# Kernel optimization log

Measured on AMD Instinct MI355X. Metric: run time of the kernel, lower is better.

The kernel has to match this reference:

```python
import jax, jax.numpy as jnp
import numpy as np

T, B, I, H = 512, 64, 512, 512

def _glorot(key, shape):
    fan_in, fan_out = shape
    std = np.sqrt(2.0 / (fan_in + fan_out))
    return (jax.random.normal(key, shape, dtype=jnp.float32) * std)

def setup_inputs() -> dict:
    key = jax.random.key(0)
    ks = jax.random.split(key, 9)
    inp = {"X": jax.random.normal(ks[0], (T, B, I), dtype=jnp.float32)}
    names = ["Wa_x", "Wi_x", "Wf_x", "Wo_x"]
    for n, k in zip(names, ks[1:5]):
        inp[n] = _glorot(k, (I, H))
    names_h = ["Wa_h", "Wi_h", "Wf_h", "Wo_h"]
    for n, k in zip(names_h, ks[5:9]):
        inp[n] = _glorot(k, (H, H))
    for n in ["ba", "bi", "bf", "bo"]:
        inp[n] = jnp.zeros((H,), dtype=jnp.float32)
    return inp

def reference(X, Wa_x, Wi_x, Wf_x, Wo_x, Wa_h, Wi_h, Wf_h, Wo_h, ba, bi, bf, bo):
    # Precompute input projections for all timesteps: [T,B,H] each
    Xa = jnp.einsum('tbi,ih->tbh', X, Wa_x) + ba
    Xi = jnp.einsum('tbi,ih->tbh', X, Wi_x) + bi
    Xf = jnp.einsum('tbi,ih->tbh', X, Wf_x) + bf
    Xo = jnp.einsum('tbi,ih->tbh', X, Wo_x) + bo

    def step(carry, xt):
        h, s = carry
        xa, xi, xf, xo = xt
        # At t=0 h=0 and s=0, which matches the original's special-cased first step
        a = jnp.tanh(xa + h @ Wa_h)
        i = jax.nn.sigmoid(xi + h @ Wi_h)
        f = jax.nn.sigmoid(xf + h @ Wf_h)
        o = jax.nn.sigmoid(xo + h @ Wo_h)
        s_new = a * i + s * f
        h_new = jnp.tanh(s_new) * o
        return (h_new, s_new), h_new

    h0 = jnp.zeros((B, H), dtype=X.dtype)
    s0 = jnp.zeros((B, H), dtype=X.dtype)
    _, hs = jax.lax.scan(step, (h0, s0), (Xa, Xi, Xf, Xo))
    return hs  # [T, B, H] (return_sequences=True)
```

## Files before the change

### kernel.cpp

```cpp
#include <hip/hip_runtime.h>
#include <cmath>


typedef __attribute__((ext_vector_type(8)))  short   short8;
typedef __attribute__((ext_vector_type(4)))  short   short4v;
typedef __attribute__((ext_vector_type(4)))  float   f32x4;
typedef __attribute__((ext_vector_type(16))) float   f32x16;

#define TSTEPS 512

__device__ __forceinline__ unsigned short f2bf(float f) {
  unsigned u = __builtin_bit_cast(unsigned, f);
  unsigned r = (u + 0x7FFFu + ((u >> 16) & 1u)) >> 16;
  return (unsigned short)r;
}
__device__ __forceinline__ float bf2f(unsigned short s) {
  unsigned u = ((unsigned)s) << 16;
  return __builtin_bit_cast(float, u);
}
__device__ __forceinline__ void gload_lds16(const void* g, void* l) {
  __builtin_amdgcn_global_load_lds(
      (const __attribute__((address_space(1))) unsigned int*)g,
      (__attribute__((address_space(3))) unsigned int*)l, 16, 0, 0);
}
__device__ __forceinline__ float sigmoid_fast(float x) {
  return 1.0f / (1.0f + __expf(-x));
}
__device__ __forceinline__ float tanh_fast(float x) {
  float e = __expf(2.0f * x);
  return 1.0f - 2.0f / (e + 1.0f);
}

__global__ __launch_bounds__(256) void prep_wT(
    const float* __restrict__ Wax, const float* __restrict__ Wix,
    const float* __restrict__ Wfx, const float* __restrict__ Wox,
    const float* __restrict__ Wah, const float* __restrict__ Wih,
    const float* __restrict__ Wfh, const float* __restrict__ Woh,
    unsigned short* __restrict__ WxT, unsigned short* __restrict__ WhT) {
  __shared__ float tile[32][33];
  int bx = blockIdx.x;
  int mat = bx >> 8;
  int t32 = bx & 255;
  int k0 = (t32 & 15) * 32;
  int h0 = (t32 >> 4) * 32;
  const float* S =
      (mat == 0) ? Wax : (mat == 1) ? Wix : (mat == 2) ? Wfx :
      (mat == 3) ? Wox : (mat == 4) ? Wah : (mat == 5) ? Wih :
      (mat == 6) ? Wfh : Woh;
  unsigned short* D = (mat < 4) ? WxT : WhT;
  int g = mat & 3;
  int tx = threadIdx.x & 31, ty = threadIdx.x >> 5;
#pragma unroll
  for (int r = 0; r < 4; ++r)
    tile[ty + r * 8][tx] = S[(size_t)(k0 + ty + r * 8) * 512 + h0 + tx];
  __syncthreads();
#pragma unroll
  for (int r = 0; r < 4; ++r) {
    int h = h0 + ty + r * 8;
    int k = k0 + tx;
    D[((size_t)(g * 512 + h) << 9) + k] = f2bf(tile[tx][ty + r * 8]);
  }
}

__global__ __launch_bounds__(256) void prep_xbf(const float* __restrict__ X,
                                                unsigned short* __restrict__ Xbf) {
  size_t i = (size_t)blockIdx.x * 256 + threadIdx.x;
  f32x4 v = *(const f32x4*)(X + i * 4);
  short4v o;
  o[0] = (short)f2bf(v[0]); o[1] = (short)f2bf(v[1]);
  o[2] = (short)f2bf(v[2]); o[3] = (short)f2bf(v[3]);
  *(short4v*)(Xbf + i * 4) = o;
}

__global__ __launch_bounds__(256) void prep_bias(
    const float* __restrict__ ba, const float* __restrict__ bi,
    const float* __restrict__ bf, const float* __restrict__ bo,
    float* __restrict__ biascat) {
  int n = blockIdx.x * 256 + threadIdx.x;
  int g = n >> 9, h = n & 511;
  const float* s = (g == 0) ? ba : (g == 1) ? bi : (g == 2) ? bf : bo;
  biascat[n] = s[h];
}

__global__ __launch_bounds__(256, 1) void lstm_fused(
    const unsigned short* __restrict__ Xbf,
    const unsigned short* __restrict__ WxT,
    const float* __restrict__ bcat,
    unsigned short* __restrict__ Xg,
    const unsigned short* __restrict__ WhT,
    unsigned short* __restrict__ hbuf,
    int* __restrict__ flags,
    int* __restrict__ xcnt,
    float* __restrict__ out) {
  __shared__ unsigned short smem[32768];
  const int tid = threadIdx.x;
  const int w = tid >> 6, l = tid & 63;

  if (blockIdx.x >= 32) {
    unsigned short* Asm_ = smem;
    unsigned short* Bsm_ = smem + 8192;
    const int wkr = blockIdx.x - 32;
    const int wm = (w >> 1) * 64, wn = (w & 1) * 64;
#pragma unroll 1
    for (int id = wkr; id < 4096; id += 512) {
      const int mt = id >> 4, nt = id & 15;
      const int m0 = mt * 128, n0 = nt * 128;
      f32x4 acc[4][4] = {};
      for (int ks = 0; ks < 8; ++ks) {
        int k0 = ks * 64;
        __syncthreads();
        int lr = l >> 3;
        int ksl = ((l & 7) ^ lr) * 8;
#pragma unroll
        for (int ii = 0; ii < 4; ++ii) {
          int i = w * 4 + ii;
          int r = i * 8 + lr;
          gload_lds16(Xbf + (size_t)(m0 + r) * 512 + k0 + ksl,
                      Asm_ + i * 512 + l * 8);
        }
#pragma unroll
        for (int ii = 0; ii < 4; ++ii) {
          int i = w * 4 + ii;
          int r = i * 8 + lr;
          gload_lds16(WxT + (size_t)(n0 + r) * 512 + k0 + ksl,
                      Bsm_ + i * 512 + l * 8);
        }
        __syncthreads();
#pragma unroll
        for (int kk = 0; kk < 2; ++kk) {
          short8 af[4], bfr[4];
#pragma unroll
          for (int mi = 0; mi < 4; ++mi) {
            int row = wm + mi * 16 + (l & 15);
            int slot = (kk * 4 + (l >> 4)) ^ (row & 7);
            af[mi] = *(const short8*)(Asm_ + row * 64 + slot * 8);
          }
#pragma unroll
          for (int ni = 0; ni < 4; ++ni) {
            int row = wn + ni * 16 + (l & 15);
            int slot = (kk * 4 + (l >> 4)) ^ (row & 7);
            bfr[ni] = *(const short8*)(Bsm_ + row * 64 + slot * 8);
          }
#pragma unroll
          for (int mi = 0; mi < 4; ++mi)
#pragma unroll
            for (int ni = 0; ni < 4; ++ni)
              acc[mi][ni] = __builtin_amdgcn_mfma_f32_16x16x32_bf16(
                  af[mi], bfr[ni], acc[mi][ni], 0, 0, 0);
        }
      }
#pragma unroll
      for (int mi = 0; mi < 4; ++mi)
#pragma unroll
        for (int ni = 0; ni < 4; ++ni) {
          int col = n0 + wn + ni * 16 + (l & 15);
          float bias = bcat[col];
          int g = col >> 9, h = col & 511;
          int chunk = h >> 3, e = h & 7;
#pragma unroll
          for (int r = 0; r < 4; ++r) {
            int m = m0 + wm + mi * 16 + (l >> 4) * 4 + r;
            int tt = m >> 6, bb = m & 63;
            unsigned off =
                (unsigned)(((((tt * 4 + g) * 64 + chunk) * 64 + bb) * 8 + e) * 2);
            unsigned val = (unsigned)f2bf(acc[mi][ni][r] + bias);
            asm volatile("global_store_short %0, %1, %2 sc0 sc1"
                         :: "v"(off), "v"(val), "s"(Xg) : "memory");
          }
        }
      asm volatile("s_waitcnt vmcnt(0)" ::: "memory");
      __syncthreads();
      if (tid == 0)
        __hip_atomic_fetch_add(xcnt + mt, 1, __ATOMIC_RELAXED,
                               __HIP_MEMORY_SCOPE_AGENT);
    }
    return;
  }

  unsigned short* hsm0 = smem;
  unsigned short* hsm1 = smem + 16384;
  const int j = blockIdx.x;
  const int mi = j & 1;
  const int cc = j >> 1;

  short8 wf[32];
  {
    const int m = l & 31;
    const int g = m >> 3;
    const int hcol_w = cc * 32 + w * 8 + (m & 7);
    const unsigned short* base =
        WhT + (((size_t)(g * 512 + hcol_w)) << 9) + (l >> 5) * 8;
#pragma unroll
    for (int kt = 0; kt < 32; ++kt) wf[kt] = *(const short8*)(base + kt * 16);
  }

  const int b = mi * 32 + (l & 31);
  const int half = l >> 5;
  const int hcol0 = cc * 32 + w * 8 + half * 4;
  const int mychunk = cc * 4 + w;

  const unsigned stg_goff0 = (unsigned)(half * 1024 + (mi * 32 + (l & 31)) * 16);
  const int stg_loff0 = w * 8192 + l * 16;
  const int ld_loff0 = half * 512 + (l & 31) * 16;
  const unsigned st_voff = (unsigned)(mychunk * 1024 + b * 16 + half * 8);

  int* const myflag = flags + (mi * 16 + cc) * 32;
  int* const pollflag = flags + (mi * 16 + (l & 15)) * 32;

  float s4[4] = {0.f, 0.f, 0.f, 0.f};

  uint2 xgn[4];
  int verified = 0;
  {
    int cv;
    do {
      cv = __hip_atomic_load(xcnt, __ATOMIC_RELAXED, __HIP_MEMORY_SCOPE_AGENT);
    } while (!__all(cv >= 16));
    asm volatile("" ::: "memory");
#pragma unroll
    for (int g = 0; g < 4; ++g)
      xgn[g] = *(const uint2*)(Xg +
          ((((size_t)(0 * 4 + g) * 64 + mychunk) * 64 + b) * 8 + half * 4));
  }

#pragma unroll 1
  for (int t = 0; t < TSTEPS; ++t) {
    f32x16 asum = {};
    if (t > 0) {
      int fv;
      do {
        fv = __hip_atomic_load(pollflag, __ATOMIC_RELAXED,
                               __HIP_MEMORY_SCOPE_AGENT);
      } while (!__all(fv >= t));
      asm volatile("" ::: "memory");
      const unsigned short* hbase = hbuf + (size_t)((t - 1) & 1) * 32768;
      unsigned short* hs = ((t - 1) & 1) ? hsm1 : hsm0;
      short8 tmp[8];
#pragma unroll
      for (int i = 0; i < 8; ++i) {
        asm volatile("global_load_dwordx4 %0, %1, %2 sc0 sc1"
                     : "=v"(tmp[i])
                     : "v"(stg_goff0 + (unsigned)((w * 8 + i) * 2048)),
                       "s"(hbase));
      }
      asm volatile("s_waitcnt vmcnt(0)" ::: "memory");
      __builtin_amdgcn_sched_barrier(0);
#pragma unroll
      for (int i = 0; i < 8; ++i)
        *(short8*)((char*)hs + stg_loff0 + i * 1024) = tmp[i];
      __syncthreads();
      f32x16 a0 = {}, a1 = {};
#pragma unroll
      for (int kt = 0; kt < 32; kt += 2) {
        short8 b0 = *(const short8*)((const char*)hs + ld_loff0 + kt * 1024);
        short8 b1 = *(const short8*)((const char*)hs + ld_loff0 + (kt + 1) * 1024);
        a0 = __builtin_amdgcn_mfma_f32_32x32x16_bf16(wf[kt], b0, a0, 0, 0, 0);
        a1 = __builtin_amdgcn_mfma_f32_32x32x16_bf16(wf[kt + 1], b1, a1,
                                                     0, 0, 0);
      }
      asum = a0 + a1;
    }
    float hout[4];
#pragma unroll
    for (int q = 0; q < 4; ++q) {
      float pa = asum[0 * 4 + q] + bf2f((unsigned short)((q < 2 ? xgn[0].x : xgn[0].y) >> ((q & 1) * 16)));
      float pi = asum[1 * 4 + q] + bf2f((unsigned short)((q < 2 ? xgn[1].x : xgn[1].y) >> ((q & 1) * 16)));
      float pf = asum[2 * 4 + q] + bf2f((unsigned short)((q < 2 ? xgn[2].x : xgn[2].y) >> ((q & 1) * 16)));
      float po = asum[3 * 4 + q] + bf2f((unsigned short)((q < 2 ? xgn[3].x : xgn[3].y) >> ((q & 1) * 16)));
      float a  = tanh_fast(pa);
      float ig = sigmoid_fast(pi);
      float fg = sigmoid_fast(pf);
      float og = sigmoid_fast(po);
      s4[q] = a * ig + s4[q] * fg;
      hout[q] = tanh_fast(s4[q]) * og;
    }
    {
      unsigned lo = (unsigned)f2bf(hout[0]) | ((unsigned)f2bf(hout[1]) << 16);
      unsigned hi = (unsigned)f2bf(hout[2]) | ((unsigned)f2bf(hout[3]) << 16);
      uint2 hd; hd.x = lo; hd.y = hi;
      const unsigned short* sbase = hbuf + (size_t)(t & 1) * 32768;
      asm volatile("global_store_dwordx2 %0, %1, %2 sc0 sc1"
                   :: "v"(st_voff), "v"(hd), "s"(sbase) : "memory");
      asm volatile("s_waitcnt vmcnt(0)" ::: "memory");
      __syncthreads();
      if (tid == 0)
        __hip_atomic_store(myflag, t + 1, __ATOMIC_RELAXED,
                           __HIP_MEMORY_SCOPE_AGENT);
    }
    f32x4 ov;
    ov[0] = hout[0]; ov[1] = hout[1]; ov[2] = hout[2]; ov[3] = hout[3];
    *(f32x4*)(out + ((size_t)t * 64 + b) * 512 + hcol0) = ov;
    const int tn = (t + 1 < TSTEPS) ? t + 1 : TSTEPS - 1;
    const int mtn = tn >> 1;
    if (mtn > verified) {
      int cv;
      do {
        cv = __hip_atomic_load(xcnt + mtn, __ATOMIC_RELAXED,
                               __HIP_MEMORY_SCOPE_AGENT);
      } while (!__all(cv >= 16));
      asm volatile("" ::: "memory");
      verified = mtn;
    }
#pragma unroll
    for (int g = 0; g < 4; ++g)
      xgn[g] = *(const uint2*)(Xg +
          ((((size_t)(tn * 4 + g) * 64 + mychunk) * 64 + b) * 8 + half * 4));
  }
}

extern "C" void kernel_launch(void* const* d_in, const int* in_sizes, int n_in,
                              void* d_out, int out_size, void* d_ws,
                              size_t ws_size, hipStream_t stream) {
  const float* X   = (const float*)d_in[0];
  const float* Wax = (const float*)d_in[1];
  const float* Wix = (const float*)d_in[2];
  const float* Wfx = (const float*)d_in[3];
  const float* Wox = (const float*)d_in[4];
  const float* Wah = (const float*)d_in[5];
  const float* Wih = (const float*)d_in[6];
  const float* Wfh = (const float*)d_in[7];
  const float* Woh = (const float*)d_in[8];
  const float* ba  = (const float*)d_in[9];
  const float* bi  = (const float*)d_in[10];
  const float* bf  = (const float*)d_in[11];
  const float* bo  = (const float*)d_in[12];

  char* ws = (char*)d_ws;
  unsigned short* Xg   = (unsigned short*)(ws);
  unsigned short* Xbf  = (unsigned short*)(ws + 134217728);
  unsigned short* WxT  = (unsigned short*)(ws + 167772160);
  unsigned short* WhT  = (unsigned short*)(ws + 169869312);
  float*          bcat = (float*)(ws + 171966464);
  int*            flags= (int*)(ws + 171974656);
  int*            xcnt = (int*)(ws + 171978752);
  unsigned short* hbuf = (unsigned short*)(ws + 171980800);

  hipMemsetAsync(ws + 171974656, 0, 4096 + 1024, stream);

  prep_wT<<<2048, 256, 0, stream>>>(Wax, Wix, Wfx, Wox, Wah, Wih, Wfh, Woh,
                                    WxT, WhT);
  prep_xbf<<<16384, 256, 0, stream>>>(X, Xbf);
  prep_bias<<<8, 256, 0, stream>>>(ba, bi, bf, bo, bcat);
  lstm_fused<<<544, 256, 0, stream>>>(Xbf, WxT, bcat, Xg, WhT, hbuf, flags,
                                      xcnt, (float*)d_out);
}
```

Measured before the change: 1.857 ms.

## Stage projection epilogue through LDS for 16-byte stores and shrink worker grid

The input-projection GEMM epilogue now writes the bf16 tile into a padded LDS buffer and then issues coalesced 16-byte global stores in the recurrence-friendly Xg layout, replacing scattered 2-byte stores. The grid drops from 544 to 256 blocks, so 224 worker blocks stride over tiles and all blocks can be co-resident alongside the 32 recurrent blocks. This is meant to cut store transaction count and to reduce contention with the latency-bound recurrence. In exchange it adds an extra LDS round trip and barrier, uses slightly more shared memory, and leaves fewer GEMM workers.

```diff
diff --git a/kernel.cpp b/kernel.cpp
--- a/kernel.cpp
+++ b/kernel.cpp
@@ -92,17 +92,18 @@
     int* __restrict__ flags,
     int* __restrict__ xcnt,
     float* __restrict__ out) {
-  __shared__ unsigned short smem[32768];
+  __shared__ unsigned short smem[33792];
   const int tid = threadIdx.x;
   const int w = tid >> 6, l = tid & 63;
 
   if (blockIdx.x >= 32) {
     unsigned short* Asm_ = smem;
     unsigned short* Bsm_ = smem + 8192;
+    unsigned short* tbuf = smem + 16384;
     const int wkr = blockIdx.x - 32;
     const int wm = (w >> 1) * 64, wn = (w & 1) * 64;
 #pragma unroll 1
-    for (int id = wkr; id < 4096; id += 512) {
+    for (int id = wkr; id < 4096; id += 224) {
       const int mt = id >> 4, nt = id & 15;
       const int m0 = mt * 128, n0 = nt * 128;
       f32x4 acc[4][4] = {};
@@ -153,21 +154,31 @@
       for (int mi = 0; mi < 4; ++mi)
 #pragma unroll
         for (int ni = 0; ni < 4; ++ni) {
-          int col = n0 + wn + ni * 16 + (l & 15);
-          float bias = bcat[col];
-          int g = col >> 9, h = col & 511;
-          int chunk = h >> 3, e = h & 7;
+          int c = wn + ni * 16 + (l & 15);
+          float bias = bcat[n0 + c];
 #pragma unroll
           for (int r = 0; r < 4; ++r) {
-            int m = m0 + wm + mi * 16 + (l >> 4) * 4 + r;
-            int tt = m >> 6, bb = m & 63;
-            unsigned off =
-                (unsigned)(((((tt * 4 + g) * 64 + chunk) * 64 + bb) * 8 + e) * 2);
-            unsigned val = (unsigned)f2bf(acc[mi][ni][r] + bias);
-            asm volatile("global_store_short %0, %1, %2 sc0 sc1"
-                         :: "v"(off), "v"(val), "s"(Xg) : "memory");
+            int m = wm + mi * 16 + (l >> 4) * 4 + r;
+            tbuf[m * 136 + c] = f2bf(acc[mi][ni][r] + bias);
           }
         }
+      __syncthreads();
+      {
+        const int g = nt >> 2;
+        const int cb = (nt & 3) * 16;
+#pragma unroll
+        for (int u = 0; u < 8; ++u) {
+          int unit = u * 256 + tid;
+          int t_i = unit >> 10;
+          int chunk_i = (unit >> 6) & 15;
+          int b_i = unit & 63;
+          short8 v = *(const short8*)(tbuf + (t_i * 64 + b_i) * 136 + chunk_i * 8);
+          unsigned off = (unsigned)(((((mt * 2 + t_i) * 4 + g) * 64 +
+                                      (cb + chunk_i)) * 64 + b_i) * 16);
+          asm volatile("global_store_dwordx4 %0, %1, %2 sc0 sc1"
+                       :: "v"(off), "v"(v), "s"(Xg) : "memory");
+        }
+      }
       asm volatile("s_waitcnt vmcnt(0)" ::: "memory");
       __syncthreads();
       if (tid == 0)
@@ -341,6 +352,6 @@
                                     WxT, WhT);
   prep_xbf<<<16384, 256, 0, stream>>>(X, Xbf);
   prep_bias<<<8, 256, 0, stream>>>(ba, bi, bf, bo, bcat);
-  lstm_fused<<<544, 256, 0, stream>>>(Xbf, WxT, bcat, Xg, WhT, hbuf, flags,
+  lstm_fused<<<256, 256, 0, stream>>>(Xbf, WxT, bcat, Xg, WhT, hbuf, flags,
                                       xcnt, (float*)d_out);
 }
```

Result: faster. 1.762 ms (-5.1%).
